# Performance work log

Hardware: AMD Instinct MI355X
Metric: run time of the kernel (lower is better)

The kernel has to match this reference:

```python
import jax, jax.numpy as jnp
import numpy as np

H = 256  # hidden_dim
NH = 4   # num_heads
HD = H // NH  # head dim


def setup_inputs() -> dict:
    key = jax.random.key(0)
    ks = jax.random.split(key, 12)
    B, TD, ID = 65536, 512, 512
    s_t = 1.0 / np.sqrt(TD)
    s_h = 1.0 / np.sqrt(H)
    s_f = 1.0 / np.sqrt(2 * H)
    return {
        "text_features": jax.random.normal(ks[0], (B, TD), jnp.float32),
        "image_features": jax.random.normal(ks[1], (B, ID), jnp.float32),
        "W_text": jax.random.uniform(ks[2], (H, TD), jnp.float32, -s_t, s_t),
        "b_text": jax.random.uniform(ks[3], (H,), jnp.float32, -s_t, s_t),
        "W_img": jax.random.uniform(ks[4], (H, ID), jnp.float32, -s_t, s_t),
        "b_img": jax.random.uniform(ks[5], (H,), jnp.float32, -s_t, s_t),
        "in_proj_w": jax.random.normal(ks[6], (3 * H, H), jnp.float32) * s_h,  # xavier-ish
        "in_proj_b": jnp.zeros((3 * H,), jnp.float32),
        "out_proj_w": jax.random.uniform(ks[7], (H, H), jnp.float32, -s_h, s_h),
        "out_proj_b": jnp.zeros((H,), jnp.float32),
        "W_fuse": jax.random.uniform(ks[8], (H, 2 * H), jnp.float32, -s_f, s_f),
        "b_fuse": jax.random.uniform(ks[9], (H,), jnp.float32, -s_f, s_f),
    }


def _mha_seq1(q_in, kv_in, in_proj_w, in_proj_b, out_proj_w, out_proj_b):
    """nn.MultiheadAttention with query seq_len=1 and kv seq_len=1 (eval mode).
    q_in, kv_in: [B, H]. Softmax over the single key is identically 1."""
    Wq, Wk, Wv = jnp.split(in_proj_w, 3, axis=0)
    bq, bk, bv = jnp.split(in_proj_b, 3, axis=0)
    q = (q_in @ Wq.T + bq).reshape(-1, NH, HD)   # [B, nh, hd]
    k = (kv_in @ Wk.T + bk).reshape(-1, NH, HD)
    v = (kv_in @ Wv.T + bv).reshape(-1, NH, HD)
    scores = jnp.einsum("bnd,bnd->bn", q, k) / np.sqrt(HD)  # [B, nh], one key
    attn = jax.nn.softmax(scores[..., None], axis=-1)       # == 1 exactly
    out = (attn * v).reshape(-1, H)                          # concat heads
    return out @ out_proj_w.T + out_proj_b


def reference(text_features, image_features, W_text, b_text, W_img, b_img,
              in_proj_w, in_proj_b, out_proj_w, out_proj_b, W_fuse, b_fuse):
    tp = text_features @ W_text.T + b_text      # [B, H]
    ip = image_features @ W_img.T + b_img       # [B, H]
    text_att = _mha_seq1(tp, ip, in_proj_w, in_proj_b, out_proj_w, out_proj_b)
    img_att = _mha_seq1(ip, tp, in_proj_w, in_proj_b, out_proj_w, out_proj_b)
    fused = jnp.concatenate([text_att, img_att], axis=1)  # [B, 2H]
    return jax.nn.relu(fused @ W_fuse.T + b_fuse)          # dropout = eval no-op
```

## Files before the change

### kernel.cpp

```cpp
#include <hip/hip_runtime.h>
#include <hip/hip_bf16.h>

typedef __attribute__((ext_vector_type(4))) float floatx4;
typedef __attribute__((ext_vector_type(2))) float floatx2;
typedef __attribute__((ext_vector_type(8))) __bf16 bf16x8;
typedef __attribute__((ext_vector_type(8))) unsigned short ushortx8;

__device__ __forceinline__ unsigned short f2bf(float x) {
    union { float f; unsigned u; } v; v.f = x;
    unsigned r = v.u + 0x7fffu + ((v.u >> 16) & 1u);
    return (unsigned short)(r >> 16);
}

__device__ __forceinline__ bf16x8 as_bf(ushortx8 v) {
    union { ushortx8 u; bf16x8 b; } x; x.u = v; return x.b;
}

__device__ __forceinline__ bf16x8 cvt8(floatx4 lo, floatx4 hi) {
    union { bf16x8 v; __hip_bfloat162 h[4]; } u;
    float2 p;
    p.x = lo.x; p.y = lo.y; u.h[0] = __float22bfloat162_rn(p);
    p.x = lo.z; p.y = lo.w; u.h[1] = __float22bfloat162_rn(p);
    p.x = hi.x; p.y = hi.y; u.h[2] = __float22bfloat162_rn(p);
    p.x = hi.z; p.y = hi.w; u.h[3] = __float22bfloat162_rn(p);
    return u.v;
}

__global__ void k1_tree(const float* __restrict__ W_fuse, const float* __restrict__ OP,
                        const float* __restrict__ ipw, const float* __restrict__ ipb,
                        const float* __restrict__ W_img, const float* __restrict__ W_text,
                        const float* __restrict__ opb, const float* __restrict__ b_img,
                        const float* __restrict__ b_text,
                        float* __restrict__ U0, float* __restrict__ U1,
                        float* __restrict__ Vimg, float* __restrict__ Vtxt,
                        float* __restrict__ vb_img, float* __restrict__ vb_txt,
                        float* __restrict__ cvec) {
    const int bid = blockIdx.x;
    const int t = threadIdx.x;
    const float* Wv = ipw + 512 * 256;
    if (bid == 96) {
        if (t < 256) {
            float a0 = opb[t], a1 = 0.f, a2 = 0.f;
            const float* oprow = OP + t * 256;
            const float* wvrow = Wv + t * 256;
            #pragma unroll 4
            for (int k = 0; k < 256; ++k) {
                a0 = fmaf(oprow[k], ipb[512 + k], a0);
                a1 = fmaf(wvrow[k], b_img[k], a1);
                a2 = fmaf(wvrow[k], b_text[k], a2);
            }
            cvec[t] = a0; vb_img[t] = a1; vb_txt[t] = a2;
        }
        return;
    }
    const float *A, *B; float* C; int lda, ldb, ldc, aoff, tm, tn;
    if (bid < 32) {
        int h = bid >> 4, tt = bid & 15;
        A = W_fuse; lda = 512; aoff = h * 256;
        B = OP; ldb = 256; C = h ? U1 : U0; ldc = 256;
        tm = tt >> 2; tn = tt & 3;
    } else {
        int b2 = bid - 32; int h = b2 >> 5; int tt = b2 & 31;
        A = Wv; lda = 256; aoff = 0;
        B = h ? W_text : W_img; ldb = 512; C = h ? Vtxt : Vimg; ldc = 512;
        tm = tt >> 3; tn = tt & 7;
    }
    __shared__ float As[16][68];
    __shared__ float Bs[16][68];
    const int arow = t >> 3, ak = (t & 7) * 2;
    const int brow = t >> 5, bc = (t & 31) * 2;
    const int ty = t >> 4, tx = t & 15;
    float acc[2][4] = {};
    for (int k0 = 0; k0 < 256; k0 += 16) {
        floatx2 av = *(const floatx2*)(A + (size_t)(tm * 64 + arow) * lda + aoff + k0 + ak);
        floatx2 bv = *(const floatx2*)(B + (size_t)(k0 + brow) * ldb + tn * 64 + bc);
        __syncthreads();
        As[ak + 0][arow] = av.x;
        As[ak + 1][arow] = av.y;
        *(floatx2*)&Bs[brow][bc] = bv;
        __syncthreads();
        #pragma unroll
        for (int kk = 0; kk < 16; ++kk) {
            floatx2 a = *(const floatx2*)&As[kk][ty * 2];
            floatx4 b = *(const floatx4*)&Bs[kk][tx * 4];
            acc[0][0] = fmaf(a.x, b.x, acc[0][0]); acc[0][1] = fmaf(a.x, b.y, acc[0][1]);
            acc[0][2] = fmaf(a.x, b.z, acc[0][2]); acc[0][3] = fmaf(a.x, b.w, acc[0][3]);
            acc[1][0] = fmaf(a.y, b.x, acc[1][0]); acc[1][1] = fmaf(a.y, b.y, acc[1][1]);
            acc[1][2] = fmaf(a.y, b.z, acc[1][2]); acc[1][3] = fmaf(a.y, b.w, acc[1][3]);
        }
    }
    #pragma unroll
    for (int i = 0; i < 2; ++i) {
        floatx4 o; o.x = acc[i][0]; o.y = acc[i][1]; o.z = acc[i][2]; o.w = acc[i][3];
        *(floatx4*)(C + (size_t)(tm * 64 + ty * 2 + i) * ldc + tn * 64 + tx * 4) = o;
    }
}

__global__ void k2_A(const float* __restrict__ U0, const float* __restrict__ U1,
                     const float* __restrict__ Vimg, const float* __restrict__ Vtxt,
                     const float* __restrict__ W_fuse, const float* __restrict__ b_fuse,
                     const float* __restrict__ vb_img, const float* __restrict__ vb_txt,
                     const float* __restrict__ cvec,
                     unsigned short* __restrict__ Wt, float* __restrict__ b_total) {
    const int bid = blockIdx.x;
    const int t = threadIdx.x;
    if (bid == 64) {
        if (t < 256) {
            float acc = b_fuse[t];
            const float* u0 = U0 + t * 256;
            const float* u1 = U1 + t * 256;
            const float* wf = W_fuse + t * 512;
            #pragma unroll 4
            for (int j = 0; j < 256; ++j) {
                acc = fmaf(u0[j], vb_img[j], acc);
                acc = fmaf(u1[j], vb_txt[j], acc);
                acc = fmaf(wf[j] + wf[j + 256], cvec[j], acc);
            }
            b_total[t] = acc;
        }
        return;
    }
    const int h = bid >> 5, tt = bid & 31;
    const float* A = h ? U1 : U0;
    const float* B = h ? Vtxt : Vimg;
    const int tm = tt >> 3, tn = tt & 7;
    __shared__ float As[16][68];
    __shared__ float Bs[16][68];
    const int arow = t >> 3, ak = (t & 7) * 2;
    const int brow = t >> 5, bc = (t & 31) * 2;
    const int n_l = t >> 3, oct = t & 7;
    float acc[8] = {};
    for (int k0 = 0; k0 < 256; k0 += 16) {
        floatx2 av = *(const floatx2*)(A + (size_t)(tm * 64 + arow) * 256 + k0 + ak);
        floatx2 bv = *(const floatx2*)(B + (size_t)(k0 + brow) * 512 + tn * 64 + bc);
        __syncthreads();
        As[ak + 0][arow] = av.x;
        As[ak + 1][arow] = av.y;
        *(floatx2*)&Bs[brow][bc] = bv;
        __syncthreads();
        #pragma unroll
        for (int kk = 0; kk < 16; ++kk) {
            float u = As[kk][n_l];
            floatx4 v0 = *(const floatx4*)&Bs[kk][oct * 8];
            floatx4 v1 = *(const floatx4*)&Bs[kk][oct * 8 + 4];
            acc[0] = fmaf(u, v0.x, acc[0]); acc[1] = fmaf(u, v0.y, acc[1]);
            acc[2] = fmaf(u, v0.z, acc[2]); acc[3] = fmaf(u, v0.w, acc[3]);
            acc[4] = fmaf(u, v1.x, acc[4]); acc[5] = fmaf(u, v1.y, acc[5]);
            acc[6] = fmaf(u, v1.z, acc[6]); acc[7] = fmaf(u, v1.w, acc[7]);
        }
    }
    const int n = tm * 64 + n_l;
    const int kg = h * 512 + tn * 64 + oct * 8;
    const int kq = kg >> 5, q = (kg >> 3) & 3;
    const int nt = n >> 4, nl = n & 15;
    union { ushortx8 v; unsigned short s[8]; } o;
    #pragma unroll
    for (int j = 0; j < 8; ++j) o.s[j] = f2bf(acc[j]);
    *(ushortx8*)&Wt[(size_t)((nt * 32 + kq) * 64 + q * 16 + nl) * 8] = o.v;
}

__global__ __launch_bounds__(256, 2)
void fused_gemm(const float* __restrict__ Ximg, const float* __restrict__ Xtxt,
                const unsigned short* __restrict__ Wt,
                const float* __restrict__ b_total, float* __restrict__ out) {
    const int bid = blockIdx.x;
    const int rowtile = bid >> 1, cb = bid & 1;
    const int t = threadIdx.x, lane = t & 63, w = t >> 6;
    const int ml = lane & 15, q = lane >> 4;
    const size_t rowbase = (size_t)rowtile * 128 + w * 32;
    const size_t roff0 = (rowbase + ml) * 512 + q * 8;
    const size_t roff1 = roff0 + (size_t)16 * 512;
    const unsigned short* wbase = Wt + ((size_t)(cb * 8) * 32) * 512 + lane * 8;

    floatx4 acc[2][8];
    #pragma unroll
    for (int mi = 0; mi < 2; ++mi)
        #pragma unroll
        for (int ni = 0; ni < 8; ++ni) acc[mi][ni] = (floatx4){0.f, 0.f, 0.f, 0.f};

    floatx4 aA[2][2], aB[2][2];

    auto loadA = [&](int idx, floatx4 (&dst)[2][2]) {
        const float* X = (idx < 16) ? Ximg : Xtxt;
        const size_t ko = (size_t)(idx & 15) * 32;
        dst[0][0] = *(const floatx4*)(X + roff0 + ko);
        dst[0][1] = *(const floatx4*)(X + roff0 + ko + 4);
        dst[1][0] = *(const floatx4*)(X + roff1 + ko);
        dst[1][1] = *(const floatx4*)(X + roff1 + ko + 4);
    };
    auto loadB = [&](int kq, ushortx8 (&bf)[8]) {
        const unsigned short* p = wbase + (size_t)kq * 512;
        #pragma unroll
        for (int ni = 0; ni < 8; ++ni) bf[ni] = *(const ushortx8*)(p + (size_t)ni * 32 * 512);
    };
    auto docompute = [&](floatx4 (&af32)[2][2], ushortx8 (&bf)[8]) {
        bf16x8 af[2];
        #pragma unroll
        for (int mi = 0; mi < 2; ++mi) af[mi] = cvt8(af32[mi][0], af32[mi][1]);
        #pragma unroll
        for (int mi = 0; mi < 2; ++mi)
            #pragma unroll
            for (int ni = 0; ni < 8; ++ni)
                acc[mi][ni] = __builtin_amdgcn_mfma_f32_16x16x32_bf16(af[mi], as_bf(bf[ni]), acc[mi][ni], 0, 0, 0);
    };

    loadA(0, aA);
    #pragma unroll 2
    for (int kq = 0; kq < 32; kq += 2) {
        ushortx8 b0[8];
        loadB(kq, b0);
        loadA(kq + 1, aB);
        docompute(aA, b0);
        ushortx8 b1[8];
        loadB(kq + 1, b1);
        loadA(kq + 2, aA);
        docompute(aB, b1);
    }

    const int colbase = cb * 128;
    #pragma unroll
    for (int ni = 0; ni < 8; ++ni) {
        const int col = colbase + ni * 16 + ml;
        const float bias = b_total[col];
        #pragma unroll
        for (int mi = 0; mi < 2; ++mi) {
            const size_t r0 = rowbase + mi * 16 + q * 4;
            #pragma unroll
            for (int e = 0; e < 4; ++e) {
                float v = acc[mi][ni][e] + bias;
                out[(r0 + e) * 256 + col] = fmaxf(v, 0.f);
            }
        }
    }
}

extern "C" void kernel_launch(void* const* d_in, const int* in_sizes, int n_in,
                              void* d_out, int out_size, void* d_ws, size_t ws_size,
                              hipStream_t stream) {
    const float* text       = (const float*)d_in[0];
    const float* image      = (const float*)d_in[1];
    const float* W_text     = (const float*)d_in[2];
    const float* b_text     = (const float*)d_in[3];
    const float* W_img      = (const float*)d_in[4];
    const float* b_img      = (const float*)d_in[5];
    const float* in_proj_w  = (const float*)d_in[6];
    const float* in_proj_b  = (const float*)d_in[7];
    const float* out_proj_w = (const float*)d_in[8];
    const float* out_proj_b = (const float*)d_in[9];
    const float* W_fuse     = (const float*)d_in[10];
    const float* b_fuse     = (const float*)d_in[11];
    float* out = (float*)d_out;

    float* ws      = (float*)d_ws;
    float* U0      = ws;
    float* U1      = ws + 65536;
    float* Vimg    = ws + 131072;
    float* Vtxt    = ws + 262144;
    float* vb_img  = ws + 393216;
    float* vb_txt  = ws + 393472;
    float* cvec    = ws + 393728;
    float* b_total = ws + 393984;
    unsigned short* Wt = (unsigned short*)(ws + 394240);

    k1_tree<<<dim3(97), dim3(512), 0, stream>>>(W_fuse, out_proj_w, in_proj_w, in_proj_b,
                                                W_img, W_text, out_proj_b, b_img, b_text,
                                                U0, U1, Vimg, Vtxt, vb_img, vb_txt, cvec);
    k2_A<<<dim3(65), dim3(512), 0, stream>>>(U0, U1, Vimg, Vtxt, W_fuse, b_fuse,
                                             vb_img, vb_txt, cvec, Wt, b_total);
    fused_gemm<<<dim3(1024), dim3(256), 0, stream>>>(image, text, Wt, b_total, out);
}
```

Before: 441.3 us.

## Stage activations through LDS with async global_load_lds double buffering

The fused GEMM now stages 32-row activation tiles through shared memory using direct global-to-LDS loads, double-buffered across four K stages with one barrier per stage. Each block covers 32 rows and all 256 output columns, each wave owning 64 columns, instead of 128 rows by 128 columns. The grid doubles to 2048 blocks. This removes the duplicate activation reads made by the two column blocks, but B-fragments are now fetched from global memory inside the inner loop with no prefetch, and the 66KB of LDS per block may limit occupancy.

After: 396.8 us. -10.1%, faster.

```diff
diff --git a/kernel.cpp b/kernel.cpp
--- a/kernel.cpp
+++ b/kernel.cpp
@@ -163,64 +163,64 @@
 void fused_gemm(const float* __restrict__ Ximg, const float* __restrict__ Xtxt,
                 const unsigned short* __restrict__ Wt,
                 const float* __restrict__ b_total, float* __restrict__ out) {
-    const int bid = blockIdx.x;
-    const int rowtile = bid >> 1, cb = bid & 1;
+    __shared__ float lds[2][32 * 260];
     const int t = threadIdx.x, lane = t & 63, w = t >> 6;
     const int ml = lane & 15, q = lane >> 4;
-    const size_t rowbase = (size_t)rowtile * 128 + w * 32;
-    const size_t roff0 = (rowbase + ml) * 512 + q * 8;
-    const size_t roff1 = roff0 + (size_t)16 * 512;
-    const unsigned short* wbase = Wt + ((size_t)(cb * 8) * 32) * 512 + lane * 8;
-
-    floatx4 acc[2][8];
+    const size_t rowbase = (size_t)blockIdx.x * 32;
+
+    floatx4 acc[2][4];
     #pragma unroll
     for (int mi = 0; mi < 2; ++mi)
         #pragma unroll
-        for (int ni = 0; ni < 8; ++ni) acc[mi][ni] = (floatx4){0.f, 0.f, 0.f, 0.f};
-
-    floatx4 aA[2][2], aB[2][2];
-
-    auto loadA = [&](int idx, floatx4 (&dst)[2][2]) {
-        const float* X = (idx < 16) ? Ximg : Xtxt;
-        const size_t ko = (size_t)(idx & 15) * 32;
-        dst[0][0] = *(const floatx4*)(X + roff0 + ko);
-        dst[0][1] = *(const floatx4*)(X + roff0 + ko + 4);
-        dst[1][0] = *(const floatx4*)(X + roff1 + ko);
-        dst[1][1] = *(const floatx4*)(X + roff1 + ko + 4);
+        for (int ni = 0; ni < 4; ++ni) acc[mi][ni] = (floatx4){0.f, 0.f, 0.f, 0.f};
+
+    auto stage = [&](int s, int b) {
+        const float* X = (s < 2) ? Ximg : Xtxt;
+        const int koff = (s & 1) * 256;
+        #pragma unroll
+        for (int i = 0; i < 8; ++i) {
+            const int r = w * 8 + i;
+            const float* gp = X + (rowbase + r) * 512 + koff + lane * 4;
+            float* lp = &lds[b][r * 260];
+            __builtin_amdgcn_global_load_lds(
+                (const __attribute__((address_space(1))) unsigned int*)gp,
+                (__attribute__((address_space(3))) unsigned int*)lp, 16, 0, 0);
+        }
     };
-    auto loadB = [&](int kq, ushortx8 (&bf)[8]) {
-        const unsigned short* p = wbase + (size_t)kq * 512;
-        #pragma unroll
-        for (int ni = 0; ni < 8; ++ni) bf[ni] = *(const ushortx8*)(p + (size_t)ni * 32 * 512);
+
+    auto compute = [&](int s, int b) {
+        #pragma unroll
+        for (int kqi = 0; kqi < 8; ++kqi) {
+            const int kq = s * 8 + kqi;
+            bf16x8 af[2];
+            #pragma unroll
+            for (int mi = 0; mi < 2; ++mi) {
+                const float* p = &lds[b][(mi * 16 + ml) * 260 + kqi * 32 + q * 8];
+                floatx4 lo = *(const floatx4*)p;
+                floatx4 hi = *(const floatx4*)(p + 4);
+                af[mi] = cvt8(lo, hi);
+            }
+            #pragma unroll
+            for (int ni = 0; ni < 4; ++ni) {
+                const int nt = w * 4 + ni;
+                ushortx8 bv = *(const ushortx8*)(Wt + (size_t)((nt * 32 + kq) * 64 + lane) * 8);
+                #pragma unroll
+                for (int mi = 0; mi < 2; ++mi)
+                    acc[mi][ni] = __builtin_amdgcn_mfma_f32_16x16x32_bf16(af[mi], as_bf(bv), acc[mi][ni], 0, 0, 0);
+            }
+        }
     };
-    auto docompute = [&](floatx4 (&af32)[2][2], ushortx8 (&bf)[8]) {
-        bf16x8 af[2];
-        #pragma unroll
-        for (int mi = 0; mi < 2; ++mi) af[mi] = cvt8(af32[mi][0], af32[mi][1]);
-        #pragma unroll
-        for (int mi = 0; mi < 2; ++mi)
-            #pragma unroll
-            for (int ni = 0; ni < 8; ++ni)
-                acc[mi][ni] = __builtin_amdgcn_mfma_f32_16x16x32_bf16(af[mi], as_bf(bf[ni]), acc[mi][ni], 0, 0, 0);
-    };
-
-    loadA(0, aA);
-    #pragma unroll 2
-    for (int kq = 0; kq < 32; kq += 2) {
-        ushortx8 b0[8];
-        loadB(kq, b0);
-        loadA(kq + 1, aB);
-        docompute(aA, b0);
-        ushortx8 b1[8];
-        loadB(kq + 1, b1);
-        loadA(kq + 2, aA);
-        docompute(aB, b1);
-    }
-
-    const int colbase = cb * 128;
-    #pragma unroll
-    for (int ni = 0; ni < 8; ++ni) {
-        const int col = colbase + ni * 16 + ml;
+
+    stage(0, 0);
+    for (int s = 0; s < 4; ++s) {
+        __syncthreads();
+        if (s < 3) stage(s + 1, (s + 1) & 1);
+        compute(s, s & 1);
+    }
+
+    #pragma unroll
+    for (int ni = 0; ni < 4; ++ni) {
+        const int col = w * 64 + ni * 16 + ml;
         const float bias = b_total[col];
         #pragma unroll
         for (int mi = 0; mi < 2; ++mi) {
@@ -267,5 +267,5 @@
                                                 U0, U1, Vimg, Vtxt, vb_img, vb_txt, cvec);
     k2_A<<<dim3(65), dim3(512), 0, stream>>>(U0, U1, Vimg, Vtxt, W_fuse, b_fuse,
                                              vb_img, vb_txt, cvec, Wt, b_total);
-    fused_gemm<<<dim3(1024), dim3(256), 0, stream>>>(image, text, Wt, b_total, out);
-}
+    fused_gemm<<<dim3(2048), dim3(256), 0, stream>>>(image, text, Wt, b_total, out);
+}
```
